# Kernel tuning notes

Hardware: AMD Instinct MI355X
Metric: run time of the kernel (lower is better)

Reference implementation:

```python
import jax, jax.numpy as jnp
import numpy as np

EPS = 1e-5  # GraphNorm eps


def setup_inputs() -> dict:
    key = jax.random.key(0)
    ks = jax.random.split(key, 8)
    B, N, D, L = 8, 2048, 128, 3
    return {
        "instance": jax.random.uniform(ks[0], (B, N, 2), jnp.float32),
        "Wn": jax.random.normal(ks[1], (D, 2), jnp.float32) * 0.5,
        "bn": jnp.zeros((D,), jnp.float32),
        "Wg": jax.random.normal(ks[2], (L, D, D), jnp.float32) / np.sqrt(D).astype(np.float32),
        "bg": jnp.zeros((L, D), jnp.float32),
        "gn_w": jnp.ones((D,), jnp.float32),
        "gn_b": jnp.zeros((D,), jnp.float32),
        "gn_a": jnp.ones((D,), jnp.float32),
    }


def reference(instance, Wn, bn, Wg, bg, gn_w, gn_b, gn_a):
    # instance: [B, N, 2] city coordinates. Graph is complete, so the PyG
    # edge-list GCN over all (i != j) pairs + self-loops is exactly a dense
    # symmetric-normalized adjacency matmul per graph.
    B, N, _ = instance.shape
    # pairwise Euclidean distances (cdist), safe sqrt to keep diagonal exact 0
    sq = jnp.sum(instance * instance, axis=-1)                      # [B, N]
    d2 = sq[:, :, None] + sq[:, None, :] - 2.0 * jnp.einsum(
        'bnd,bmd->bnm', instance, instance)                          # [B, N, N]
    pos = d2 > 0
    dist = jnp.where(pos, jnp.sqrt(jnp.where(pos, d2, 1.0)), 0.0)    # [B, N, N]
    # GCN edge weights = distances, self-loops added with weight 1.0
    A = dist + jnp.eye(N, dtype=dist.dtype)
    deg = jnp.sum(A, axis=-1)                                        # [B, N]
    dinv = jax.lax.rsqrt(deg)
    An = dinv[:, :, None] * A * dinv[:, None, :]                     # D^-1/2 A D^-1/2

    h = jnp.einsum('bne,de->bnd', instance, Wn) + bn                 # proj_node
    for l in range(Wg.shape[0]):
        # GCNConv: aggregate normalized messages of lin(x), then bias
        hw = jnp.einsum('bnm,bmd->bnd', An, jnp.einsum('bnd,ed->bne', h, Wg[l])) + bg[l]
        h = jnp.tanh(hw) + h                                         # activation + residual
        # GraphNorm (shared params across layers): per-graph, per-feature stats
        mean = jnp.mean(h, axis=1, keepdims=True)                    # [B, 1, D]
        sub = h - gn_a * mean
        var = jnp.mean(sub * sub, axis=1, keepdims=True)
        h = gn_w * sub * jax.lax.rsqrt(var + EPS) + gn_b
    return h  # [B, N, D] (unbatch+stack of equal-size graphs)
```

## Files before the change

kernel.cpp:

```cpp
#include <hip/hip_runtime.h>
#include <hip/hip_bf16.h>
#include <math.h>

#define BB 8
#define NN 2048
#define DD 128
#define LL 3
#define GN_EPS 1e-5f

typedef __attribute__((ext_vector_type(8))) short bf16x8;
typedef __attribute__((ext_vector_type(4))) float f32x4;
typedef __attribute__((ext_vector_type(8))) unsigned short u16x8;

#define FSQRT(x) __builtin_amdgcn_sqrtf(x)

#define GLL16(gp, lp) __builtin_amdgcn_global_load_lds( \
    (const __attribute__((address_space(1))) void*)(gp), \
    (__attribute__((address_space(3))) void*)(lp), 16, 0, 0)

#define WAIT_VM12 0x0F7C

__device__ __forceinline__ unsigned short f2bf(float f) {
    union { float f; unsigned u; } v; v.f = f;
    return (unsigned short)((v.u + 0x8000u) >> 16);
}

__device__ __forceinline__ float fast_tanh(float x) {
    float e = __expf(-2.0f * fabsf(x));
    float t = (1.0f - e) * __builtin_amdgcn_rcpf(1.0f + e);
    return copysignf(t, x);
}

__device__ __forceinline__ void stats_sc(float ps, float pq, float a, float w_,
                                         float b_, float& s, float& c) {
    const float inv_n = 1.0f / (float)NN;
    float mean = ps * inv_n;
    float msq  = pq * inv_n;
    float var  = msq - mean * mean * a * (2.0f - a);
    float rstd = rsqrtf(var + GN_EPS);
    s = w_ * rstd;
    c = b_ - s * (a * mean);
}


__global__ __launch_bounds__(256)
void prep_wg(const float* __restrict__ Wg, const float* __restrict__ Wn,
             const float* __restrict__ bn, unsigned short* __restrict__ wgf,
             float* __restrict__ weff, float* __restrict__ beff)
{
    const int f = blockIdx.x * 256 + threadIdx.x;
    const int l  = f >> 14;
    const int r  = f & 16383;
    const int dp = r >> 7;
    const int e  = r & 127;
    const int dpt = dp >> 4, ll = dp & 15;
    const int kc  = e >> 5,  eo = e & 31;
    wgf[((((l * 8 + dpt) * 4 + kc) * 16 + ll) << 5) + eo] = f2bf(Wg[f]);

    if (blockIdx.x == 0 && threadIdx.x < 128) {
        const int ee = threadIdx.x;
        float a0 = 0.f, a1 = 0.f, cc = 0.f;
        for (int d = 0; d < 128; ++d) {
            const float wv = Wg[ee * 128 + d];
            a0 = fmaf(wv, Wn[d * 2 + 0], a0);
            a1 = fmaf(wv, Wn[d * 2 + 1], a1);
            cc = fmaf(wv, bn[d], cc);
        }
        weff[ee * 2 + 0] = a0;
        weff[ee * 2 + 1] = a1;
        beff[ee] = cc;
    }
}

__global__ __launch_bounds__(256)
void gen_pack(const float* __restrict__ inst, const float* __restrict__ Wn,
              const float* __restrict__ bn, const float* __restrict__ weff,
              const float* __restrict__ beff, unsigned short* __restrict__ Ap,
              float* __restrict__ dinv, float* __restrict__ h,
              unsigned short* __restrict__ tp,
              float* __restrict__ psum, float* __restrict__ psq)
{
    __shared__ float cs[NN * 2];
    __shared__ float part[4][16];
    const int b     = blockIdx.x & 7;
    const int ntile = blockIdx.x >> 3;
    const int n0    = ntile * 16;
    const int tid   = threadIdx.x;
    const int w     = tid >> 6;
    const int lane  = tid & 63;
    const int lq    = lane >> 4;
    const int ll    = lane & 15;

    const float* instb = inst + b * NN * 2;
    for (int i = tid; i < (NN * 2) / 4; i += 256)
        ((float4*)cs)[i] = ((const float4*)instb)[i];
    __syncthreads();

    const int n = n0 + ll;
    const float nx = cs[n * 2 + 0];
    const float ny = cs[n * 2 + 1];

    u16x8* apw = (u16x8*)Ap + (size_t)(b * 128 + ntile) * 64 * 64 + (w * 16) * 64 + lane;

    const int diagkcg = ntile >> 1;
    float rs = 0.f;
    for (int kc = 0; kc < 16; ++kc) {
        const int kcg = w * 16 + kc;
        const int mb  = kcg * 32 + lq * 8;
        const float* cp = &cs[mb * 2];
        float4 c01 = *(const float4*)(cp + 0);
        float4 c23 = *(const float4*)(cp + 4);
        float4 c45 = *(const float4*)(cp + 8);
        float4 c67 = *(const float4*)(cp + 12);
        float mxx[8] = { c01.x, c01.z, c23.x, c23.z, c45.x, c45.z, c67.x, c67.z };
        float myy[8] = { c01.y, c01.w, c23.y, c23.w, c45.y, c45.w, c67.y, c67.w };
        float dist[8];
        #pragma unroll
        for (int j = 0; j < 8; ++j) {
            float dx = nx - mxx[j];
            float dy = ny - myy[j];
            dist[j] = FSQRT(dx * dx + dy * dy);
        }
        if (kcg == diagkcg) {
            #pragma unroll
            for (int j = 0; j < 8; ++j)
                if (mb + j == n) dist[j] = 1.0f;
        }
        u16x8 pk;
        #pragma unroll
        for (int j = 0; j < 8; ++j) {
            pk[j] = f2bf(dist[j]);
            rs += dist[j];
        }
        apw[kc * 64] = pk;
    }

    rs += __shfl_xor(rs, 16);
    rs += __shfl_xor(rs, 32);
    if (lq == 0) part[w][ll] = rs;
    __syncthreads();
    if (tid < 16)
        dinv[b * NN + n0 + tid] = rsqrtf(part[0][tid] + part[1][tid] +
                                         part[2][tid] + part[3][tid]);

    {
        const int d  = tid & 127;
        const int r0 = tid >> 7;
        const float w0 = Wn[d * 2 + 0];
        const float w1 = Wn[d * 2 + 1];
        const float bv = bn[d];
        const float we0 = weff[d * 2 + 0];
        const float we1 = weff[d * 2 + 1];
        const float be  = beff[d];
        const int kcg   = ntile >> 1;
        const int mbase = (ntile & 1) * 16;
        const int dt    = d >> 4;
        const int lld   = d & 15;
        unsigned short* tpd =
            tp + (((size_t)(b * 64 + kcg) * 8 + dt) * 64 + lld) * 8;
        #pragma unroll
        for (int r = r0; r < 16; r += 2) {
            const float x0 = cs[(n0 + r) * 2 + 0];
            const float x1 = cs[(n0 + r) * 2 + 1];
            h[((size_t)b * NN + n0 + r) * DD + d] = fmaf(x0, w0, fmaf(x1, w1, bv));
            const float dv = rsqrtf(part[0][r] + part[1][r] + part[2][r] + part[3][r]);
            const int mloc = mbase + r;
            const int lqa  = mloc >> 3;
            const int j    = mloc & 7;
            tpd[(size_t)lqa * 128 + j] = f2bf(dv * fmaf(x0, we0, fmaf(x1, we1, be)));
        }
    }
    if (blockIdx.x == 0) {
        for (int i = tid; i < LL * BB * DD; i += 256) { psum[i] = 0.f; psq[i] = 0.f; }
    }
}

template <bool HP>
__global__ __launch_bounds__(256)
void lin_mfma(const float* __restrict__ h, const unsigned short* __restrict__ wgf_l,
              const float* __restrict__ dinv,
              const float* __restrict__ psumP, const float* __restrict__ psqP,
              const float* __restrict__ ga, const float* __restrict__ gw,
              const float* __restrict__ gb, unsigned short* __restrict__ tp)
{
    __shared__ float sL[DD], cL[DD];
    const int tid  = threadIdx.x;
    const int b    = blockIdx.x & 7;
    const int tile = blockIdx.x >> 3;
    const int row0 = b * NN + tile * 32;
    const int w    = tid >> 6;
    const int lane = tid & 63;
    const int lq   = lane >> 4;
    const int ll   = lane & 15;

    if (tid < DD) {
        float s = 1.0f, c = 0.0f;
        if (HP)
            stats_sc(psumP[b * DD + tid], psqP[b * DD + tid],
                     ga[tid], gw[tid], gb[tid], s, c);
        sL[tid] = s; cL[tid] = c;
    }
    __syncthreads();

    bf16x8 aw[2][4];
    #pragma unroll
    for (int mt = 0; mt < 2; ++mt) {
        const int dpt = 2 * w + mt;
        #pragma unroll
        for (int kc = 0; kc < 4; ++kc)
            aw[mt][kc] = *(const bf16x8*)&wgf_l[(((dpt * 4 + kc) * 16 + ll) << 5) + lq * 8];
    }

    bf16x8 bh[2][4];
    #pragma unroll
    for (int nt = 0; nt < 2; ++nt) {
        const float* hrow = h + (size_t)(row0 + nt * 16 + ll) * DD;
        #pragma unroll
        for (int kc = 0; kc < 4; ++kc) {
            float4 h0 = *(const float4*)&hrow[kc * 32 + lq * 8];
            float4 h1 = *(const float4*)&hrow[kc * 32 + lq * 8 + 4];
            const int e0 = kc * 32 + lq * 8;
            bf16x8 p;
            p[0] = (short)f2bf(fmaf(sL[e0 + 0], h0.x, cL[e0 + 0]));
            p[1] = (short)f2bf(fmaf(sL[e0 + 1], h0.y, cL[e0 + 1]));
            p[2] = (short)f2bf(fmaf(sL[e0 + 2], h0.z, cL[e0 + 2]));
            p[3] = (short)f2bf(fmaf(sL[e0 + 3], h0.w, cL[e0 + 3]));
            p[4] = (short)f2bf(fmaf(sL[e0 + 4], h1.x, cL[e0 + 4]));
            p[5] = (short)f2bf(fmaf(sL[e0 + 5], h1.y, cL[e0 + 5]));
            p[6] = (short)f2bf(fmaf(sL[e0 + 6], h1.z, cL[e0 + 6]));
            p[7] = (short)f2bf(fmaf(sL[e0 + 7], h1.w, cL[e0 + 7]));
            bh[nt][kc] = p;
        }
    }

    f32x4 acc[2][2];
    #pragma unroll
    for (int i = 0; i < 2; ++i)
        #pragma unroll
        for (int j = 0; j < 2; ++j) acc[i][j] = (f32x4)0.0f;

    #pragma unroll
    for (int kc = 0; kc < 4; ++kc)
        #pragma unroll
        for (int nt = 0; nt < 2; ++nt)
            #pragma unroll
            for (int mt = 0; mt < 2; ++mt)
                acc[nt][mt] = __builtin_amdgcn_mfma_f32_16x16x32_bf16(
                    bh[nt][kc], aw[mt][kc], acc[nt][mt], 0, 0, 0);

    #pragma unroll
    for (int nt = 0; nt < 2; ++nt) {
        const int mloc0 = nt * 16 + lq * 4;
        const int lq_a  = mloc0 >> 3;
        const int j0    = mloc0 & 7;
        float4 di4 = *(const float4*)&dinv[row0 + mloc0];
        #pragma unroll
        for (int mt = 0; mt < 2; ++mt) {
            const int dt = 2 * w + mt;
            ushort4 pk;
            pk.x = f2bf(acc[nt][mt][0] * di4.x);
            pk.y = f2bf(acc[nt][mt][1] * di4.y);
            pk.z = f2bf(acc[nt][mt][2] * di4.z);
            pk.w = f2bf(acc[nt][mt][3] * di4.w);
            *(ushort4*)&tp[((size_t)((b * 64 + tile) * 8 + dt) * 64 + lq_a * 16 + ll) * 8 + j0] = pk;
        }
    }
}

template <bool HP>
__global__ __launch_bounds__(256, 2)
void agg_mfma(const unsigned short* __restrict__ Ap, const unsigned short* __restrict__ tp,
              const float* __restrict__ dinv, const float* __restrict__ bg_l,
              const float* __restrict__ psumP, const float* __restrict__ psqP,
              const float* __restrict__ ga, const float* __restrict__ gw,
              const float* __restrict__ gb,
              float* __restrict__ h, float* __restrict__ psum, float* __restrict__ psq)
{
    __shared__ char Abuf[7][8192];
    const int b     = blockIdx.x & 7;
    const int t2    = blockIdx.x >> 3;
    const int n0    = t2 * 32;
    const int tid   = threadIdx.x;
    const int w     = tid >> 6;
    const int lane  = tid & 63;
    const int lq    = lane >> 4;
    const int ll    = lane & 15;

    const unsigned short* apsrc = Ap + ((size_t)(b * 128 + t2 * 2) * 64) * 512 + lane * 8;
    const unsigned short* tpb   = tp + ((size_t)b * 64 * 8) * 512 + lane * 8;

    f32x4 acc[2][2];
    acc[0][0] = (f32x4)0.0f; acc[0][1] = (f32x4)0.0f;
    acc[1][0] = (f32x4)0.0f; acc[1][1] = (f32x4)0.0f;

    bf16x8 fb[3][2][4];

#define GLLA(c) { \
        GLL16(apsrc + (size_t)((((c) & 15) * 4 + w)) * 512, \
              &Abuf[(c) % 7][w * 1024]); \
        GLL16(apsrc + (size_t)((((c) & 15) * 4 + w)) * 512 + 32768, \
              &Abuf[(c) % 7][4096 + w * 1024]); \
    }
#define LOADB(c) { \
        const int kb_ = ((c) & 15) * 4; \
        _Pragma("unroll") \
        for (int s_ = 0; s_ < 4; ++s_) { \
            fb[(c) % 3][0][s_] = *(const bf16x8*)(tpb + (size_t)((kb_ + s_) * 8 + 2 * w + 0) * 512); \
            fb[(c) % 3][1][s_] = *(const bf16x8*)(tpb + (size_t)((kb_ + s_) * 8 + 2 * w + 1) * 512); \
        } \
    }

    GLLA(0) GLLA(1) GLLA(2) GLLA(3)
    LOADB(0)
    GLLA(4)
    LOADB(1)
    GLLA(5)

    #pragma unroll
    for (int k = 0; k < 16; ++k) {
        __builtin_amdgcn_s_waitcnt(WAIT_VM12);
        __builtin_amdgcn_s_barrier();
        __builtin_amdgcn_sched_barrier(0);
        bf16x8 af[2][4];
        const char* lb = &Abuf[k % 7][0];
        #pragma unroll
        for (int nt = 0; nt < 2; ++nt)
            #pragma unroll
            for (int s = 0; s < 4; ++s)
                af[nt][s] = *(const bf16x8*)(lb + nt * 4096 + s * 1024 + lane * 16);
        LOADB(k + 2)
        GLLA(k + 6)
        __builtin_amdgcn_sched_barrier(0);
        #pragma unroll
        for (int s = 0; s < 4; ++s) {
            #pragma unroll
            for (int nt = 0; nt < 2; ++nt) {
                acc[nt][0] = __builtin_amdgcn_mfma_f32_16x16x32_bf16(fb[k % 3][0][s], af[nt][s], acc[nt][0], 0, 0, 0);
                acc[nt][1] = __builtin_amdgcn_mfma_f32_16x16x32_bf16(fb[k % 3][1][s], af[nt][s], acc[nt][1], 0, 0, 0);
            }
        }
    }
#undef GLLA
#undef LOADB

    const float di0 = dinv[b * NN + n0 + ll];
    const float di1 = dinv[b * NN + n0 + 16 + ll];
    #pragma unroll
    for (int dtl = 0; dtl < 2; ++dtl) {
        const int d0 = (2 * w + dtl) * 16 + lq * 4;
        float4 bg4 = *(const float4*)&bg_l[d0];
        float sres[4] = {1.f, 1.f, 1.f, 1.f}, cres[4] = {0.f, 0.f, 0.f, 0.f};
        if (HP) {
            float4 ps4 = *(const float4*)&psumP[b * DD + d0];
            float4 pq4 = *(const float4*)&psqP[b * DD + d0];
            float4 ga4 = *(const float4*)&ga[d0];
            float4 gw4 = *(const float4*)&gw[d0];
            float4 gb4 = *(const float4*)&gb[d0];
            stats_sc(ps4.x, pq4.x, ga4.x, gw4.x, gb4.x, sres[0], cres[0]);
            stats_sc(ps4.y, pq4.y, ga4.y, gw4.y, gb4.y, sres[1], cres[1]);
            stats_sc(ps4.z, pq4.z, ga4.z, gw4.z, gb4.z, sres[2], cres[2]);
            stats_sc(ps4.w, pq4.w, ga4.w, gw4.w, gb4.w, sres[3], cres[3]);
        }
        float hs[4] = {0.f, 0.f, 0.f, 0.f}, hq[4] = {0.f, 0.f, 0.f, 0.f};
        #pragma unroll
        for (int nt = 0; nt < 2; ++nt) {
            const int n = n0 + nt * 16 + ll;
            const float di = nt ? di1 : di0;
            size_t idx = ((size_t)b * NN + n) * DD + d0;
            float4 hv = *(const float4*)&h[idx];
            float outv[4];
            #pragma unroll
            for (int r = 0; r < 4; ++r) {
                float pre = di * acc[nt][dtl][r] + (&bg4.x)[r];
                outv[r] = fast_tanh(pre) + fmaf(sres[r], (&hv.x)[r], cres[r]);
                hs[r] += outv[r];
                hq[r] += outv[r] * outv[r];
            }
            float4 ov = { outv[0], outv[1], outv[2], outv[3] };
            *(float4*)&h[idx] = ov;
        }

        #pragma unroll
        for (int off = 1; off < 16; off <<= 1) {
            #pragma unroll
            for (int r = 0; r < 4; ++r) {
                hs[r] += __shfl_xor(hs[r], off);
                hq[r] += __shfl_xor(hq[r], off);
            }
        }
        if (ll == 0) {
            #pragma unroll
            for (int r = 0; r < 4; ++r) {
                atomicAdd(&psum[b * DD + d0 + r], hs[r]);
                atomicAdd(&psq[b * DD + d0 + r], hq[r]);
            }
        }
    }
}

__global__ __launch_bounds__(256)
void apply_kernel(const float* __restrict__ h,
                  const float* __restrict__ psum2, const float* __restrict__ psq2,
                  const float* __restrict__ ga, const float* __restrict__ gw,
                  const float* __restrict__ gb, float* __restrict__ dst)
{
    const int i4 = blockIdx.x * 256 + threadIdx.x;
    const int dg = (i4 & 31) * 4;
    const int b  = i4 >> 16;
    float4 hv = ((const float4*)h)[i4];
    float o[4];
    #pragma unroll
    for (int j = 0; j < 4; ++j) {
        const int d = dg + j;
        float s, c;
        stats_sc(psum2[b * DD + d], psq2[b * DD + d], ga[d], gw[d], gb[d], s, c);
        o[j] = fmaf(s, (&hv.x)[j], c);
    }
    float4 ov = { o[0], o[1], o[2], o[3] };
    ((float4*)dst)[i4] = ov;
}

extern "C" void kernel_launch(void* const* d_in, const int* in_sizes, int n_in,
                              void* d_out, int out_size, void* d_ws, size_t ws_size,
                              hipStream_t stream)
{
    const float* inst = (const float*)d_in[0];
    const float* Wn   = (const float*)d_in[1];
    const float* bn   = (const float*)d_in[2];
    const float* Wg   = (const float*)d_in[3];
    const float* bg   = (const float*)d_in[4];
    const float* gw   = (const float*)d_in[5];
    const float* gb   = (const float*)d_in[6];
    const float* ga   = (const float*)d_in[7];
    float* out = (float*)d_out;

    float* ws   = (float*)d_ws;
    float* dinv = ws;
    float* h    = dinv + BB * NN;
    float* psum = h + (size_t)BB * NN * DD;
    float* psq  = psum + LL * BB * DD;
    float* weff = psq + LL * BB * DD;
    float* beff = weff + 2 * DD;
    unsigned short* wgf = (unsigned short*)(beff + DD);
    unsigned short* tp  = wgf + LL * DD * DD;
    unsigned short* Ap  = tp + (size_t)BB * DD * NN;

    prep_wg<<<(LL * DD * DD) / 256, 256, 0, stream>>>(Wg, Wn, bn, wgf, weff, beff);
    gen_pack<<<1024, 256, 0, stream>>>(inst, Wn, bn, weff, beff, Ap, dinv, h, tp, psum, psq);

    agg_mfma<false><<<512, 256, 0, stream>>>(
        Ap, tp, dinv, bg + 0 * DD, nullptr, nullptr, ga, gw, gb, h, psum, psq);

    for (int l = 1; l < LL; ++l) {
        const unsigned short* wgl = wgf + (size_t)l * DD * DD;
        const float* psP = psum + (size_t)(l - 1) * BB * DD;
        const float* pqP = psq  + (size_t)(l - 1) * BB * DD;
        float* psL = psum + (size_t)l * BB * DD;
        float* pqL = psq  + (size_t)l * BB * DD;
        lin_mfma<true><<<(BB * NN) / 32, 256, 0, stream>>>(
            h, wgl, dinv, psP, pqP, ga, gw, gb, tp);
        agg_mfma<true><<<512, 256, 0, stream>>>(
            Ap, tp, dinv, bg + l * DD, psP, pqP, ga, gw, gb, h, psL, pqL);
    }
    apply_kernel<<<(BB * NN * DD / 4) / 256, 256, 0, stream>>>(
        h, psum + 2 * BB * DD, psq + 2 * BB * DD, ga, gw, gb, out);
}
```

Before: 186.8 us.

## Recompute distance adjacency on the fly in aggregation instead of storing it

The dense bf16 distance matrix is no longer materialized in global memory. Each aggregation block loads the graph's coordinates into shared memory and regenerates the adjacency fragments per k-step, using double-buffered LDS with a block barrier per iteration. This removes the 64 MB write of the matrix plus its repeated reads across three layers. In exchange it adds sqrt and ALU work to the MFMA loop and swaps the deep async global_load_lds pipeline for simpler synchronous double buffering.

```diff
diff --git a/kernel.cpp b/kernel.cpp
--- a/kernel.cpp
+++ b/kernel.cpp
@@ -13,12 +13,6 @@
 typedef __attribute__((ext_vector_type(8))) unsigned short u16x8;
 
 #define FSQRT(x) __builtin_amdgcn_sqrtf(x)
-
-#define GLL16(gp, lp) __builtin_amdgcn_global_load_lds( \
-    (const __attribute__((address_space(1))) void*)(gp), \
-    (__attribute__((address_space(3))) void*)(lp), 16, 0, 0)
-
-#define WAIT_VM12 0x0F7C
 
 __device__ __forceinline__ unsigned short f2bf(float f) {
     union { float f; unsigned u; } v; v.f = f;
@@ -75,7 +69,7 @@
 __global__ __launch_bounds__(256)
 void gen_pack(const float* __restrict__ inst, const float* __restrict__ Wn,
               const float* __restrict__ bn, const float* __restrict__ weff,
-              const float* __restrict__ beff, unsigned short* __restrict__ Ap,
+              const float* __restrict__ beff,
               float* __restrict__ dinv, float* __restrict__ h,
               unsigned short* __restrict__ tp,
               float* __restrict__ psum, float* __restrict__ psq)
@@ -99,8 +93,6 @@
     const int n = n0 + ll;
     const float nx = cs[n * 2 + 0];
     const float ny = cs[n * 2 + 1];
-
-    u16x8* apw = (u16x8*)Ap + (size_t)(b * 128 + ntile) * 64 * 64 + (w * 16) * 64 + lane;
 
     const int diagkcg = ntile >> 1;
     float rs = 0.f;
@@ -126,13 +118,8 @@
             for (int j = 0; j < 8; ++j)
                 if (mb + j == n) dist[j] = 1.0f;
         }
-        u16x8 pk;
-        #pragma unroll
-        for (int j = 0; j < 8; ++j) {
-            pk[j] = f2bf(dist[j]);
-            rs += dist[j];
-        }
-        apw[kc * 64] = pk;
+        #pragma unroll
+        for (int j = 0; j < 8; ++j) rs += dist[j];
     }
 
     rs += __shfl_xor(rs, 16);
@@ -269,78 +256,107 @@
 
 template <bool HP>
 __global__ __launch_bounds__(256, 2)
-void agg_mfma(const unsigned short* __restrict__ Ap, const unsigned short* __restrict__ tp,
+void agg_mfma(const float* __restrict__ inst, const unsigned short* __restrict__ tp,
               const float* __restrict__ dinv, const float* __restrict__ bg_l,
               const float* __restrict__ psumP, const float* __restrict__ psqP,
               const float* __restrict__ ga, const float* __restrict__ gw,
               const float* __restrict__ gb,
               float* __restrict__ h, float* __restrict__ psum, float* __restrict__ psq)
 {
-    __shared__ char Abuf[7][8192];
-    const int b     = blockIdx.x & 7;
-    const int t2    = blockIdx.x >> 3;
-    const int n0    = t2 * 32;
-    const int tid   = threadIdx.x;
-    const int w     = tid >> 6;
-    const int lane  = tid & 63;
-    const int lq    = lane >> 4;
-    const int ll    = lane & 15;
-
-    const unsigned short* apsrc = Ap + ((size_t)(b * 128 + t2 * 2) * 64) * 512 + lane * 8;
-    const unsigned short* tpb   = tp + ((size_t)b * 64 * 8) * 512 + lane * 8;
+    __shared__ float cs[NN * 2];
+    __shared__ char Abuf[2][8192];
+    const int b    = blockIdx.x & 7;
+    const int t2   = blockIdx.x >> 3;
+    const int n0   = t2 * 32;
+    const int tid  = threadIdx.x;
+    const int w    = tid >> 6;
+    const int lane = tid & 63;
+    const int lq   = lane >> 4;
+    const int ll   = lane & 15;
+
+    const float* instb = inst + b * NN * 2;
+    for (int i = tid; i < (NN * 2) / 4; i += 256)
+        ((float4*)cs)[i] = ((const float4*)instb)[i];
+
+    const unsigned short* tpb = tp + ((size_t)b * 64 * 8) * 512 + lane * 8;
 
     f32x4 acc[2][2];
     acc[0][0] = (f32x4)0.0f; acc[0][1] = (f32x4)0.0f;
     acc[1][0] = (f32x4)0.0f; acc[1][1] = (f32x4)0.0f;
 
-    bf16x8 fb[3][2][4];
-
-#define GLLA(c) { \
-        GLL16(apsrc + (size_t)((((c) & 15) * 4 + w)) * 512, \
-              &Abuf[(c) % 7][w * 1024]); \
-        GLL16(apsrc + (size_t)((((c) & 15) * 4 + w)) * 512 + 32768, \
-              &Abuf[(c) % 7][4096 + w * 1024]); \
+    bf16x8 fb[2][2][4];
+
+    __syncthreads();
+
+    const int ntw  = w >> 1;
+    const int s0w  = (w & 1) * 2;
+    const int nw   = n0 + ntw * 16 + ll;
+    const float nxw = cs[nw * 2 + 0];
+    const float nyw = cs[nw * 2 + 1];
+    const int diagkcg = (n0 + ntw * 16) >> 5;
+
+#define MKFRAGS(kk) { \
+        char* wb = &Abuf[(kk) & 1][0]; \
+        _Pragma("unroll") \
+        for (int si = 0; si < 2; ++si) { \
+            const int s_   = s0w + si; \
+            const int kcg_ = (kk) * 4 + s_; \
+            const int mb_  = kcg_ * 32 + lq * 8; \
+            const float* cp_ = &cs[mb_ * 2]; \
+            float4 c01 = *(const float4*)(cp_ + 0); \
+            float4 c23 = *(const float4*)(cp_ + 4); \
+            float4 c45 = *(const float4*)(cp_ + 8); \
+            float4 c67 = *(const float4*)(cp_ + 12); \
+            float mxx[8] = { c01.x, c01.z, c23.x, c23.z, c45.x, c45.z, c67.x, c67.z }; \
+            float myy[8] = { c01.y, c01.w, c23.y, c23.w, c45.y, c45.w, c67.y, c67.w }; \
+            u16x8 pk; \
+            _Pragma("unroll") \
+            for (int j = 0; j < 8; ++j) { \
+                float dx = nxw - mxx[j]; \
+                float dy = nyw - myy[j]; \
+                float dv = FSQRT(dx * dx + dy * dy); \
+                if (kcg_ == diagkcg && mb_ + j == nw) dv = 1.0f; \
+                pk[j] = f2bf(dv); \
+            } \
+            *(u16x8*)(wb + (2 * w + si) * 1024 + lane * 16) = pk; \
+        } \
     }
 #define LOADB(c) { \
-        const int kb_ = ((c) & 15) * 4; \
+        const int kb_ = (c) * 4; \
         _Pragma("unroll") \
         for (int s_ = 0; s_ < 4; ++s_) { \
-            fb[(c) % 3][0][s_] = *(const bf16x8*)(tpb + (size_t)((kb_ + s_) * 8 + 2 * w + 0) * 512); \
-            fb[(c) % 3][1][s_] = *(const bf16x8*)(tpb + (size_t)((kb_ + s_) * 8 + 2 * w + 1) * 512); \
+            fb[(c) & 1][0][s_] = *(const bf16x8*)(tpb + (size_t)((kb_ + s_) * 8 + 2 * w + 0) * 512); \
+            fb[(c) & 1][1][s_] = *(const bf16x8*)(tpb + (size_t)((kb_ + s_) * 8 + 2 * w + 1) * 512); \
         } \
     }
 
-    GLLA(0) GLLA(1) GLLA(2) GLLA(3)
+    MKFRAGS(0)
     LOADB(0)
-    GLLA(4)
-    LOADB(1)
-    GLLA(5)
+    __syncthreads();
 
     #pragma unroll
     for (int k = 0; k < 16; ++k) {
-        __builtin_amdgcn_s_waitcnt(WAIT_VM12);
-        __builtin_amdgcn_s_barrier();
-        __builtin_amdgcn_sched_barrier(0);
         bf16x8 af[2][4];
-        const char* lb = &Abuf[k % 7][0];
+        const char* lb = &Abuf[k & 1][0];
         #pragma unroll
         for (int nt = 0; nt < 2; ++nt)
             #pragma unroll
             for (int s = 0; s < 4; ++s)
-                af[nt][s] = *(const bf16x8*)(lb + nt * 4096 + s * 1024 + lane * 16);
-        LOADB(k + 2)
-        GLLA(k + 6)
-        __builtin_amdgcn_sched_barrier(0);
-        #pragma unroll
-        for (int s = 0; s < 4; ++s) {
+                af[nt][s] = *(const bf16x8*)(lb + (nt * 4 + s) * 1024 + lane * 16);
+        if (k < 15) {
+            LOADB(k + 1)
+            MKFRAGS(k + 1)
+        }
+        #pragma unroll
+        for (int s = 0; s < 4; ++s)
             #pragma unroll
             for (int nt = 0; nt < 2; ++nt) {
-                acc[nt][0] = __builtin_amdgcn_mfma_f32_16x16x32_bf16(fb[k % 3][0][s], af[nt][s], acc[nt][0], 0, 0, 0);
-                acc[nt][1] = __builtin_amdgcn_mfma_f32_16x16x32_bf16(fb[k % 3][1][s], af[nt][s], acc[nt][1], 0, 0, 0);
+                acc[nt][0] = __builtin_amdgcn_mfma_f32_16x16x32_bf16(fb[k & 1][0][s], af[nt][s], acc[nt][0], 0, 0, 0);
+                acc[nt][1] = __builtin_amdgcn_mfma_f32_16x16x32_bf16(fb[k & 1][1][s], af[nt][s], acc[nt][1], 0, 0, 0);
             }
-        }
-    }
-#undef GLLA
+        __syncthreads();
+    }
+#undef MKFRAGS
 #undef LOADB
 
     const float di0 = dinv[b * NN + n0 + ll];
@@ -443,13 +459,12 @@
     float* beff = weff + 2 * DD;
     unsigned short* wgf = (unsigned short*)(beff + DD);
     unsigned short* tp  = wgf + LL * DD * DD;
-    unsigned short* Ap  = tp + (size_t)BB * DD * NN;
 
     prep_wg<<<(LL * DD * DD) / 256, 256, 0, stream>>>(Wg, Wn, bn, wgf, weff, beff);
-    gen_pack<<<1024, 256, 0, stream>>>(inst, Wn, bn, weff, beff, Ap, dinv, h, tp, psum, psq);
+    gen_pack<<<1024, 256, 0, stream>>>(inst, Wn, bn, weff, beff, dinv, h, tp, psum, psq);
 
     agg_mfma<false><<<512, 256, 0, stream>>>(
-        Ap, tp, dinv, bg + 0 * DD, nullptr, nullptr, ga, gw, gb, h, psum, psq);
+        inst, tp, dinv, bg + 0 * DD, nullptr, nullptr, ga, gw, gb, h, psum, psq);
 
     for (int l = 1; l < LL; ++l) {
         const unsigned short* wgl = wgf + (size_t)l * DD * DD;
@@ -460,7 +475,7 @@
         lin_mfma<true><<<(BB * NN) / 32, 256, 0, stream>>>(
             h, wgl, dinv, psP, pqP, ga, gw, gb, tp);
         agg_mfma<true><<<512, 256, 0, stream>>>(
-            Ap, tp, dinv, bg + l * DD, psP, pqP, ga, gw, gb, h, psL, pqL);
+            inst, tp, dinv, bg + l * DD, psP, pqP, ga, gw, gb, h, psL, pqL);
     }
     apply_kernel<<<(BB * NN * DD / 4) / 256, 256, 0, stream>>>(
         h, psum + 2 * BB * DD, psq + 2 * BB * DD, ga, gw, gb, out);
```

Measured after the change: 189.9 us. No clear change (+1.7%).
